# Kernel optimization log

Hardware: AMD Instinct MI355X
Metric: run time of the kernel (lower is better)

The kernel has to match this reference:

```python
import jax, jax.numpy as jnp
import numpy as np

N_HEAD = 8
T_THRESHOLD = 0.001


def setup_inputs() -> dict:
    key = jax.random.key(0)
    ks = jax.random.split(key, 5)
    B, N, NL, R = 4, 1024, 4, 256
    C = NL * R
    x = jax.random.normal(ks[0], (B, N, NL, R), dtype=jnp.float32)
    Wc = jax.random.normal(ks[1], (R, 3 * R), dtype=jnp.float32) * (1.0 / np.sqrt(R))
    bc = jnp.zeros((3 * R,), dtype=jnp.float32)
    Wp = jax.random.normal(ks[2], (C, C), dtype=jnp.float32) * (1.0 / np.sqrt(C))
    bp = jnp.zeros((C,), dtype=jnp.float32)
    return {"x": x, "Wc": Wc, "bc": bc, "Wp": Wp, "bp": bp}


def reference(x, Wc, bc, Wp, bp):
    B, N, NL, R = x.shape
    H = N_HEAD
    D = R // H  # head dim
    # shared per-level qkv projection: (B, N, NL, 3R)
    qkv = x @ Wc + bc
    q, k, v = jnp.split(qkv, 3, axis=-1)
    # split heads: (B, N, NL, H, D)
    q = q.reshape(B, N, NL, H, D)
    k = k.reshape(B, N, NL, H, D)
    v = v.reshape(B, N, NL, H, D)
    scale = 1.0 / np.sqrt(D).astype(np.float32)
    # per-level attention scores: (B, NL, H, N, N)
    att = jnp.einsum('bnlhd,bmlhd->blhnm', q, k) * scale
    att = jax.nn.softmax(att, axis=-1)
    # custom post-softmax thresholding (ReLU(softmax - T)); dropout is identity at eval
    att = jax.nn.relu(att - T_THRESHOLD)
    # multiply attentions across levels: low parent attention dooms the child
    comb = jnp.prod(att, axis=1)  # (B, H, N, N)
    # apply combined attention to each level's values: (B, N, NL, H, D)
    y = jnp.einsum('bhnm,bmlhd->bnlhd', comb, v)
    y = y.reshape(B, N, NL * H * D)  # (B, N, C)
    y = y @ Wp + bp  # c_proj; resid dropout identity at eval
    return y.reshape(B, N, NL, R)
```

## Files before the change

### kernel.cpp

```cpp
#include <hip/hip_runtime.h>

#define TTHR 0.001f
#define QSCALE 0.17677669529663687f
#define CAP 16
#define YSCALE 8388608.0f
#define YINV   1.1920928955078125e-07f

typedef _Float16 half4v __attribute__((ext_vector_type(4)));
typedef _Float16 half8v __attribute__((ext_vector_type(8)));
typedef float f32x4 __attribute__((ext_vector_type(4)));

__device__ __forceinline__ void stage_tile_s(const _Float16* __restrict__ gsrc,
                                             int rowstride, _Float16* lds, int tid)
{
  const int lane = tid & 63;
  const int w4 = (tid >> 6) << 2;
#pragma unroll
  for (int r = 0; r < 4; ++r) {
    const int p = (w4 + r) * 64 + lane;
    const int row = p >> 3, xg = p & 7;
    __builtin_amdgcn_global_load_lds(
        (const __attribute__((address_space(1))) void*)(gsrc + row * rowstride + ((xg ^ (row & 7)) << 3)),
        (__attribute__((address_space(3))) void*)(lds + (w4 + r) * 512),
        16, 0, 0);
  }
}

__global__ __launch_bounds__(256) void k_split_rm(
    const float* __restrict__ in, _Float16* __restrict__ oh,
    _Float16* __restrict__ ol, int n4)
{
  const int i = blockIdx.x * 256 + threadIdx.x;
  if (i >= n4) return;
  float4 v = ((const float4*)in)[i];
  half4v h = {(_Float16)v.x, (_Float16)v.y, (_Float16)v.z, (_Float16)v.w};
  half4v l = {(_Float16)(v.x - (float)h[0]), (_Float16)(v.y - (float)h[1]),
              (_Float16)(v.z - (float)h[2]), (_Float16)(v.w - (float)h[3])};
  ((half4v*)oh)[i] = h;
  ((half4v*)ol)[i] = l;
}

__global__ __launch_bounds__(256) void k_split_tr(
    const float* __restrict__ in, _Float16* __restrict__ oh,
    _Float16* __restrict__ ol, int K, int N)
{
  __shared__ float t[32][33];
  const int nb = N >> 5;
  const int n0 = (blockIdx.x % nb) << 5, k0 = (blockIdx.x / nb) << 5;
  const int r = threadIdx.x >> 3, c4 = (threadIdx.x & 7) << 2;
  float4 v = *(const float4*)&in[(k0 + r) * N + n0 + c4];
  t[r][c4] = v.x; t[r][c4 + 1] = v.y; t[r][c4 + 2] = v.z; t[r][c4 + 3] = v.w;
  __syncthreads();
  float a0 = t[c4][r], a1 = t[c4 + 1][r], a2 = t[c4 + 2][r], a3 = t[c4 + 3][r];
  half4v h = {(_Float16)a0, (_Float16)a1, (_Float16)a2, (_Float16)a3};
  half4v l = {(_Float16)(a0 - (float)h[0]), (_Float16)(a1 - (float)h[1]),
              (_Float16)(a2 - (float)h[2]), (_Float16)(a3 - (float)h[3])};
  *(half4v*)&oh[(n0 + r) * K + k0 + c4] = h;
  *(half4v*)&ol[(n0 + r) * K + k0 + c4] = l;
}

template<int EPI>
__global__ __launch_bounds__(256) void k_gemm_split(
    const _Float16* __restrict__ Ah, const _Float16* __restrict__ Al,
    const _Float16* __restrict__ Bh, const _Float16* __restrict__ Bl,
    const float* __restrict__ bias, int K, int kclog, int nbn,
    float* __restrict__ out, _Float16* __restrict__ Qs,
    _Float16* __restrict__ Ks, float* __restrict__ Vp)
{
  __shared__ __align__(16) _Float16 Asm[2][8192];
  __shared__ __align__(16) _Float16 Bsm[2][8192];
  const int tid = threadIdx.x, lane = tid & 63, w = tid >> 6;
  const int wr = w >> 1, wc = w & 1;
  const int lrow = lane & 15, lk = lane >> 4;
  const int mt = blockIdx.x / nbn, ct = blockIdx.x % nbn;
  const int m0 = mt << 7, c0 = ct << 7;

  const int nch = 3 << kclog;
  const int kcm = (1 << kclog) - 1;
  stage_tile_s(Ah + (size_t)m0 * K, K, Asm[0], tid);
  stage_tile_s(Bh + (size_t)c0 * K, K, Bsm[0], tid);
  __syncthreads();

  f32x4 acc[4][4] = {};
#pragma unroll 1
  for (int ch = 0; ch < nch; ++ch) {
    const int cur = ch & 1;
    if (ch + 1 < nch) {
      const int ch2 = ch + 1;
      const int phase = ch2 >> kclog, kc = ch2 & kcm;
      const _Float16* As = (phase == 2) ? Al : Ah;
      const _Float16* Bs = (phase == 1) ? Bl : Bh;
      stage_tile_s(As + (size_t)m0 * K + (kc << 6), K, Asm[cur ^ 1], tid);
      stage_tile_s(Bs + (size_t)c0 * K + (kc << 6), K, Bsm[cur ^ 1], tid);
    }
#pragma unroll
    for (int ks = 0; ks < 2; ++ks) {
      half8v af[4], bf[4];
#pragma unroll
      for (int mi = 0; mi < 4; ++mi) {
        const int row = (wr << 6) + (mi << 4) + lrow;
        const int xg = ((ks << 2) + lk) ^ (row & 7);
        af[mi] = *(const half8v*)&Asm[cur][((row << 3) + xg) << 3];
      }
#pragma unroll
      for (int ni = 0; ni < 4; ++ni) {
        const int col = (wc << 6) + (ni << 4) + lrow;
        const int xg = ((ks << 2) + lk) ^ (col & 7);
        bf[ni] = *(const half8v*)&Bsm[cur][((col << 3) + xg) << 3];
      }
#pragma unroll
      for (int mi = 0; mi < 4; ++mi)
#pragma unroll
        for (int ni = 0; ni < 4; ++ni)
          acc[mi][ni] = __builtin_amdgcn_mfma_f32_16x16x32_f16(af[mi], bf[ni], acc[mi][ni], 0, 0, 0);
    }
    __syncthreads();
  }

#pragma unroll
  for (int ni = 0; ni < 4; ++ni) {
    const int c = c0 + (wc << 6) + (ni << 4) + lrow;
    const float bv = bias[c];
    if (EPI == 0) {
#pragma unroll
      for (int mi = 0; mi < 4; ++mi)
#pragma unroll
        for (int reg = 0; reg < 4; ++reg) {
          const int m = m0 + (wr << 6) + (mi << 4) + (lk << 2) + reg;
          out[m * 1024 + c] = acc[mi][ni][reg] * YINV + bv;
        }
    } else {
      const int part = c >> 8, cc = c & 255;
      const int h = cc >> 5, d = cc & 31;
#pragma unroll
      for (int mi = 0; mi < 4; ++mi)
#pragma unroll
        for (int reg = 0; reg < 4; ++reg) {
          const int m = m0 + (wr << 6) + (mi << 4) + (lk << 2) + reg;
          const int b = m >> 12, n = (m >> 2) & 1023, l = m & 3;
          const int panel = b * 32 + l * 8 + h;
          float v = acc[mi][ni][reg] + bv;
          if (part == 2) {
            Vp[(panel << 15) + n * 32 + d] = v;
          } else {
            _Float16* dst = part ? Ks : Qs;
            if (!part) v *= QSCALE;
            _Float16 hv = (_Float16)v;
            _Float16 lv = (_Float16)(v - (float)hv);
            dst[(panel << 16) + n * 64 + d] = hv;
            dst[(panel << 16) + n * 64 + 32 + d] = lv;
          }
        }
    }
  }
}

__global__ __launch_bounds__(256) void k_score_sum(
    const _Float16* __restrict__ Qs, const _Float16* __restrict__ Ks,
    float* __restrict__ Z)
{
  __shared__ __align__(16) _Float16 Qsm[8192];
  __shared__ __align__(16) _Float16 Ksm[2][8192];
  __shared__ float Zsh[128];
  const int tid = threadIdx.x, lane = tid & 63, w = tid >> 6;
  const int wr = w >> 1, wc = w & 1;
  const int lrow = lane & 15, lk = lane >> 4;
  const int rt = blockIdx.x & 7, panel = blockIdx.x >> 3;

  stage_tile_s(Qs + (panel << 16) + (rt << 13), 64, Qsm, tid);
  stage_tile_s(Ks + (panel << 16), 64, Ksm[0], tid);
  if (tid < 128) Zsh[tid] = 0.0f;
  __syncthreads();

  const int kstA[3] = {0, 0, 4}, kstB[3] = {0, 4, 0};
  half8v af[3][4];
#pragma unroll
  for (int ks = 0; ks < 3; ++ks)
#pragma unroll
    for (int mi = 0; mi < 4; ++mi) {
      const int row = (wr << 6) + (mi << 4) + lrow;
      const int xg = (kstA[ks] + lk) ^ (row & 7);
      af[ks][mi] = *(const half8v*)&Qsm[((row << 3) + xg) << 3];
    }

  float rsum[4][4] = {};
#pragma unroll 1
  for (int ct = 0; ct < 8; ++ct) {
    const int cur = ct & 1;
    if (ct < 7)
      stage_tile_s(Ks + (panel << 16) + ((ct + 1) << 13), 64, Ksm[cur ^ 1], tid);
    f32x4 acc[4][4] = {};
#pragma unroll
    for (int ks = 0; ks < 3; ++ks) {
      half8v bf[4];
#pragma unroll
      for (int ni = 0; ni < 4; ++ni) {
        const int col = (wc << 6) + (ni << 4) + lrow;
        const int xg = (kstB[ks] + lk) ^ (col & 7);
        bf[ni] = *(const half8v*)&Ksm[cur][((col << 3) + xg) << 3];
      }
#pragma unroll
      for (int mi = 0; mi < 4; ++mi)
#pragma unroll
        for (int ni = 0; ni < 4; ++ni)
          acc[mi][ni] = __builtin_amdgcn_mfma_f32_16x16x32_f16(af[ks][mi], bf[ni], acc[mi][ni], 0, 0, 0);
    }
#pragma unroll
    for (int mi = 0; mi < 4; ++mi)
#pragma unroll
      for (int reg = 0; reg < 4; ++reg)
#pragma unroll
        for (int ni = 0; ni < 4; ++ni)
          rsum[mi][reg] += __expf(acc[mi][ni][reg]);
    __syncthreads();
  }

#pragma unroll
  for (int mi = 0; mi < 4; ++mi)
#pragma unroll
    for (int reg = 0; reg < 4; ++reg) {
      float s = rsum[mi][reg];
      s += __shfl_xor(s, 1, 64);
      s += __shfl_xor(s, 2, 64);
      s += __shfl_xor(s, 4, 64);
      s += __shfl_xor(s, 8, 64);
      if (lrow == 0) atomicAdd(&Zsh[(wr << 6) + (mi << 4) + (lk << 2) + reg], s);
    }
  __syncthreads();
  if (tid < 128) Z[panel * 1024 + (rt << 7) + tid] = Zsh[tid];
}

__global__ __launch_bounds__(256) void k_comb2(
    const _Float16* __restrict__ Qs, const _Float16* __restrict__ Ks,
    const float* __restrict__ Z, int* __restrict__ ccnt,
    unsigned short* __restrict__ cidx, float* __restrict__ cval)
{
  __shared__ __align__(16) _Float16 Asm[2][8192];
  __shared__ __align__(16) _Float16 Bsm[2][8192];
  __shared__ float tzl[2][128];
  __shared__ float rzl[128];
  __shared__ int lcnt[128];
  const int tid = threadIdx.x, lane = tid & 63, w = tid >> 6;
  const int wr = w >> 1, wc = w & 1;
  const int lrow = lane & 15, lk = lane >> 4;
  const int bid = blockIdx.x;
  const int ct = bid & 7, rt = (bid >> 3) & 7, bh = bid >> 6;
  const int b = bh >> 3, h = bh & 7;

  if (tid < 128) {
    lcnt[tid] = 0;
    const float* zp = Z + (b * 32 + h) * 1024 + (rt << 7) + tid;
    float z0 = zp[0], z1 = zp[8192], z2 = zp[16384], z3 = zp[24576];
    rzl[tid] = 1.0f / ((z0 * z1) * (z2 * z3));
    tzl[0][tid] = TTHR * z0;
  }
  {
    const int panel = b * 32 + h;
    stage_tile_s(Qs + (panel << 16) + (rt << 13), 64, Asm[0], tid);
    stage_tile_s(Ks + (panel << 16) + (ct << 13), 64, Bsm[0], tid);
  }
  __syncthreads();

  float prod[4][4][4];
#pragma unroll
  for (int mi = 0; mi < 4; ++mi)
#pragma unroll
    for (int ni = 0; ni < 4; ++ni)
#pragma unroll
      for (int r = 0; r < 4; ++r) prod[mi][ni][r] = 1.0f;

  const int kstA[3] = {0, 0, 4}, kstB[3] = {0, 4, 0};
#pragma unroll 1
  for (int l = 0; l < 4; ++l) {
    const int cur = l & 1;
    if (l < 3) {
      const int panel = b * 32 + (l + 1) * 8 + h;
      stage_tile_s(Qs + (panel << 16) + (rt << 13), 64, Asm[cur ^ 1], tid);
      stage_tile_s(Ks + (panel << 16) + (ct << 13), 64, Bsm[cur ^ 1], tid);
      if (tid < 128) tzl[cur ^ 1][tid] = TTHR * Z[panel * 1024 + (rt << 7) + tid];
    }

    f32x4 acc[4][4] = {};
#pragma unroll
    for (int ks = 0; ks < 3; ++ks) {
      half8v af[4], bf[4];
#pragma unroll
      for (int mi = 0; mi < 4; ++mi) {
        const int row = (wr << 6) + (mi << 4) + lrow;
        const int xg = (kstA[ks] + lk) ^ (row & 7);
        af[mi] = *(const half8v*)&Asm[cur][((row << 3) + xg) << 3];
      }
#pragma unroll
      for (int ni = 0; ni < 4; ++ni) {
        const int col = (wc << 6) + (ni << 4) + lrow;
        const int xg = (kstB[ks] + lk) ^ (col & 7);
        bf[ni] = *(const half8v*)&Bsm[cur][((col << 3) + xg) << 3];
      }
#pragma unroll
      for (int mi = 0; mi < 4; ++mi)
#pragma unroll
        for (int ni = 0; ni < 4; ++ni)
          acc[mi][ni] = __builtin_amdgcn_mfma_f32_16x16x32_f16(af[mi], bf[ni], acc[mi][ni], 0, 0, 0);
    }

#pragma unroll
    for (int mi = 0; mi < 4; ++mi)
#pragma unroll
      for (int reg = 0; reg < 4; ++reg) {
        const float tz = tzl[cur][(wr << 6) + (mi << 4) + (lk << 2) + reg];
#pragma unroll
        for (int ni = 0; ni < 4; ++ni) {
          const float e = __expf(acc[mi][ni][reg]) - tz;
          prod[mi][ni][reg] *= fmaxf(e, 0.0f);
        }
      }
    __syncthreads();
  }

#pragma unroll
  for (int mi = 0; mi < 4; ++mi)
#pragma unroll
    for (int ni = 0; ni < 4; ++ni)
#pragma unroll
      for (int reg = 0; reg < 4; ++reg) {
        const int rloc = (wr << 6) + (mi << 4) + (lk << 2) + reg;
        const float v = prod[mi][ni][reg] * rzl[rloc];
        if (v > 0.0f) {
          const int slot = atomicAdd(&lcnt[rloc], 1);
          if (slot < CAP) {
            const int rowc = (bh << 10) + (rt << 7) + rloc;
            const int mglob = (ct << 7) + (wc << 6) + (ni << 4) + lrow;
            cidx[(rowc * 8 + ct) * CAP + slot] = (unsigned short)mglob;
            cval[(rowc * 8 + ct) * CAP + slot] = v * YSCALE;
          }
        }
      }
  __syncthreads();
  if (tid < 128) {
    const int rowc = (bh << 10) + (rt << 7) + tid;
    ccnt[rowc * 8 + ct] = min(lcnt[tid], CAP);
  }
}

__global__ __launch_bounds__(64) void k_pv(
    const float* __restrict__ Vp, const int* __restrict__ ccnt,
    const unsigned short* __restrict__ cidx, const float* __restrict__ cval,
    _Float16* __restrict__ ysh, _Float16* __restrict__ ysl)
{
  const int rowc = blockIdx.x;
  const int bh = rowc >> 10, n = rowc & 1023;
  const int b = bh >> 3, h = bh & 7;
  const int l0 = threadIdx.x >> 5, d = threadIdx.x & 31;
  const float* vA = Vp + ((b * 32 + l0 * 8 + h) << 15) + d;
  const float* vB = vA + (16 << 15);
  float y0 = 0.f, y1 = 0.f;
  for (int mcj = 0; mcj < 8; ++mcj) {
    const int cnt = ccnt[rowc * 8 + mcj];
    const int off = (rowc * 8 + mcj) * CAP;
    for (int i = 0; i < cnt; ++i) {
      const int m = cidx[off + i];
      const float w = cval[off + i];
      y0 = fmaf(w, vA[m * 32], y0);
      y1 = fmaf(w, vB[m * 32], y1);
    }
  }
  const int idx = ((b << 10) + n) * 1024 + l0 * 256 + h * 32 + d;
  _Float16 h0 = (_Float16)y0;
  ysh[idx] = h0;
  ysl[idx] = (_Float16)(y0 - (float)h0);
  _Float16 h1 = (_Float16)y1;
  ysh[idx + 512] = h1;
  ysl[idx + 512] = (_Float16)(y1 - (float)h1);
}

extern "C" void kernel_launch(void* const* d_in, const int* in_sizes, int n_in,
                              void* d_out, int out_size, void* d_ws, size_t ws_size,
                              hipStream_t stream)
{
  const float* x  = (const float*)d_in[0];
  const float* Wc = (const float*)d_in[1];
  const float* bc = (const float*)d_in[2];
  const float* Wp = (const float*)d_in[3];
  const float* bp = (const float*)d_in[4];
  float* out = (float*)d_out;
  (void)in_sizes; (void)n_in; (void)out_size;

  if (ws_size < 98828288ull) return;
  char* wsb = (char*)d_ws;
  float*          Vp   = (float*)wsb;
  _Float16*       Qs   = (_Float16*)(wsb + 16777216);
  _Float16*       Ks   = (_Float16*)(wsb + 33554432);
  float*          Z    = (float*)(wsb + 50331648);
  _Float16*       xh   = (_Float16*)(wsb + 50855936);
  _Float16*       xl   = (_Float16*)(wsb + 59244544);
  int*            ccnt = (int*)(wsb + 67633152);
  unsigned short* cidx = (unsigned short*)(wsb + 68681728);
  float*          cval = (float*)(wsb + 77070336);
  _Float16*       Wch  = (_Float16*)(wsb + 93847552);
  _Float16*       Wcl  = (_Float16*)(wsb + 94240768);
  _Float16*       Wph  = (_Float16*)(wsb + 94633984);
  _Float16*       Wpl  = (_Float16*)(wsb + 96731136);

  k_split_rm<<<dim3(4096), dim3(256), 0, stream>>>(x, xh, xl, 1048576);
  k_split_tr<<<dim3(192), dim3(256), 0, stream>>>(Wc, Wch, Wcl, 256, 768);
  k_split_tr<<<dim3(1024), dim3(256), 0, stream>>>(Wp, Wph, Wpl, 1024, 1024);
  k_gemm_split<1><<<dim3(768), dim3(256), 0, stream>>>(
      xh, xl, Wch, Wcl, bc, 256, 2, 6, nullptr, Qs, Ks, Vp);
  k_score_sum<<<dim3(1024), dim3(256), 0, stream>>>(Qs, Ks, Z);
  k_comb2<<<dim3(2048), dim3(256), 0, stream>>>(Qs, Ks, Z, ccnt, cidx, cval);
  k_pv<<<dim3(32768), dim3(64), 0, stream>>>(Vp, ccnt, cidx, cval, xh, xl);
  k_gemm_split<0><<<dim3(256), dim3(256), 0, stream>>>(
      xh, xl, Wph, Wpl, bp, 1024, 4, 8, out, nullptr, nullptr, nullptr);
}
```

Baseline: 236.7 us.

## Halve GEMM N-tile, add XCD-aware block remap, single-buffer comb2 LDS

```diff
diff --git a/kernel.cpp b/kernel.cpp
--- a/kernel.cpp
+++ b/kernel.cpp
@@ -9,6 +9,10 @@
 typedef _Float16 half4v __attribute__((ext_vector_type(4)));
 typedef _Float16 half8v __attribute__((ext_vector_type(8)));
 typedef float f32x4 __attribute__((ext_vector_type(4)));
+
+__device__ __forceinline__ int xcd_bid() {
+  return (blockIdx.x & 7) * ((int)gridDim.x >> 3) + ((int)blockIdx.x >> 3);
+}
 
 __device__ __forceinline__ void stage_tile_s(const _Float16* __restrict__ gsrc,
                                              int rowstride, _Float16* lds, int tid)
@@ -22,6 +26,22 @@
     __builtin_amdgcn_global_load_lds(
         (const __attribute__((address_space(1))) void*)(gsrc + row * rowstride + ((xg ^ (row & 7)) << 3)),
         (__attribute__((address_space(3))) void*)(lds + (w4 + r) * 512),
+        16, 0, 0);
+  }
+}
+
+__device__ __forceinline__ void stage_tile64(const _Float16* __restrict__ gsrc,
+                                             int rowstride, _Float16* lds, int tid)
+{
+  const int lane = tid & 63;
+  const int w2 = (tid >> 6) << 1;
+#pragma unroll
+  for (int r = 0; r < 2; ++r) {
+    const int p = (w2 + r) * 64 + lane;
+    const int row = p >> 3, xg = p & 7;
+    __builtin_amdgcn_global_load_lds(
+        (const __attribute__((address_space(1))) void*)(gsrc + row * rowstride + ((xg ^ (row & 7)) << 3)),
+        (__attribute__((address_space(3))) void*)(lds + (w2 + r) * 512),
         16, 0, 0);
   }
 }
@@ -68,20 +88,21 @@
     _Float16* __restrict__ Ks, float* __restrict__ Vp)
 {
   __shared__ __align__(16) _Float16 Asm[2][8192];
-  __shared__ __align__(16) _Float16 Bsm[2][8192];
+  __shared__ __align__(16) _Float16 Bsm[2][4096];
   const int tid = threadIdx.x, lane = tid & 63, w = tid >> 6;
   const int wr = w >> 1, wc = w & 1;
   const int lrow = lane & 15, lk = lane >> 4;
-  const int mt = blockIdx.x / nbn, ct = blockIdx.x % nbn;
-  const int m0 = mt << 7, c0 = ct << 7;
+  const int bid = xcd_bid();
+  const int mt = bid / nbn, ct = bid % nbn;
+  const int m0 = mt << 7, c0 = ct << 6;
 
   const int nch = 3 << kclog;
   const int kcm = (1 << kclog) - 1;
   stage_tile_s(Ah + (size_t)m0 * K, K, Asm[0], tid);
-  stage_tile_s(Bh + (size_t)c0 * K, K, Bsm[0], tid);
-  __syncthreads();
-
-  f32x4 acc[4][4] = {};
+  stage_tile64(Bh + (size_t)c0 * K, K, Bsm[0], tid);
+  __syncthreads();
+
+  f32x4 acc[4][2] = {};
 #pragma unroll 1
   for (int ch = 0; ch < nch; ++ch) {
     const int cur = ch & 1;
@@ -91,11 +112,11 @@
       const _Float16* As = (phase == 2) ? Al : Ah;
       const _Float16* Bs = (phase == 1) ? Bl : Bh;
       stage_tile_s(As + (size_t)m0 * K + (kc << 6), K, Asm[cur ^ 1], tid);
-      stage_tile_s(Bs + (size_t)c0 * K + (kc << 6), K, Bsm[cur ^ 1], tid);
+      stage_tile64(Bs + (size_t)c0 * K + (kc << 6), K, Bsm[cur ^ 1], tid);
     }
 #pragma unroll
     for (int ks = 0; ks < 2; ++ks) {
-      half8v af[4], bf[4];
+      half8v af[4], bf[2];
 #pragma unroll
       for (int mi = 0; mi < 4; ++mi) {
         const int row = (wr << 6) + (mi << 4) + lrow;
@@ -103,23 +124,23 @@
         af[mi] = *(const half8v*)&Asm[cur][((row << 3) + xg) << 3];
       }
 #pragma unroll
-      for (int ni = 0; ni < 4; ++ni) {
-        const int col = (wc << 6) + (ni << 4) + lrow;
+      for (int ni = 0; ni < 2; ++ni) {
+        const int col = (wc << 5) + (ni << 4) + lrow;
         const int xg = ((ks << 2) + lk) ^ (col & 7);
         bf[ni] = *(const half8v*)&Bsm[cur][((col << 3) + xg) << 3];
       }
 #pragma unroll
       for (int mi = 0; mi < 4; ++mi)
 #pragma unroll
-        for (int ni = 0; ni < 4; ++ni)
+        for (int ni = 0; ni < 2; ++ni)
           acc[mi][ni] = __builtin_amdgcn_mfma_f32_16x16x32_f16(af[mi], bf[ni], acc[mi][ni], 0, 0, 0);
     }
     __syncthreads();
   }
 
 #pragma unroll
-  for (int ni = 0; ni < 4; ++ni) {
-    const int c = c0 + (wc << 6) + (ni << 4) + lrow;
+  for (int ni = 0; ni < 2; ++ni) {
+    const int c = c0 + (wc << 5) + (ni << 4) + lrow;
     const float bv = bias[c];
     if (EPI == 0) {
 #pragma unroll
@@ -165,7 +186,8 @@
   const int tid = threadIdx.x, lane = tid & 63, w = tid >> 6;
   const int wr = w >> 1, wc = w & 1;
   const int lrow = lane & 15, lk = lane >> 4;
-  const int rt = blockIdx.x & 7, panel = blockIdx.x >> 3;
+  const int bid = xcd_bid();
+  const int rt = bid & 7, panel = bid >> 3;
 
   stage_tile_s(Qs + (panel << 16) + (rt << 13), 64, Qsm, tid);
   stage_tile_s(Ks + (panel << 16), 64, Ksm[0], tid);
@@ -235,15 +257,15 @@
     const float* __restrict__ Z, int* __restrict__ ccnt,
     unsigned short* __restrict__ cidx, float* __restrict__ cval)
 {
-  __shared__ __align__(16) _Float16 Asm[2][8192];
-  __shared__ __align__(16) _Float16 Bsm[2][8192];
+  __shared__ __align__(16) _Float16 Asm[8192];
+  __shared__ __align__(16) _Float16 Bsm[8192];
   __shared__ float tzl[2][128];
   __shared__ float rzl[128];
   __shared__ int lcnt[128];
   const int tid = threadIdx.x, lane = tid & 63, w = tid >> 6;
   const int wr = w >> 1, wc = w & 1;
   const int lrow = lane & 15, lk = lane >> 4;
-  const int bid = blockIdx.x;
+  const int bid = xcd_bid();
   const int ct = bid & 7, rt = (bid >> 3) & 7, bh = bid >> 6;
   const int b = bh >> 3, h = bh & 7;
 
@@ -256,8 +278,8 @@
   }
   {
     const int panel = b * 32 + h;
-    stage_tile_s(Qs + (panel << 16) + (rt << 13), 64, Asm[0], tid);
-    stage_tile_s(Ks + (panel << 16) + (ct << 13), 64, Bsm[0], tid);
+    stage_tile_s(Qs + (panel << 16) + (rt << 13), 64, Asm, tid);
+    stage_tile_s(Ks + (panel << 16) + (ct << 13), 64, Bsm, tid);
   }
   __syncthreads();
 
@@ -272,14 +294,6 @@
   const int kstA[3] = {0, 0, 4}, kstB[3] = {0, 4, 0};
 #pragma unroll 1
   for (int l = 0; l < 4; ++l) {
-    const int cur = l & 1;
-    if (l < 3) {
-      const int panel = b * 32 + (l + 1) * 8 + h;
-      stage_tile_s(Qs + (panel << 16) + (rt << 13), 64, Asm[cur ^ 1], tid);
-      stage_tile_s(Ks + (panel << 16) + (ct << 13), 64, Bsm[cur ^ 1], tid);
-      if (tid < 128) tzl[cur ^ 1][tid] = TTHR * Z[panel * 1024 + (rt << 7) + tid];
-    }
-
     f32x4 acc[4][4] = {};
 #pragma unroll
     for (int ks = 0; ks < 3; ++ks) {
@@ -288,13 +302,13 @@
       for (int mi = 0; mi < 4; ++mi) {
         const int row = (wr << 6) + (mi << 4) + lrow;
         const int xg = (kstA[ks] + lk) ^ (row & 7);
-        af[mi] = *(const half8v*)&Asm[cur][((row << 3) + xg) << 3];
+        af[mi] = *(const half8v*)&Asm[((row << 3) + xg) << 3];
       }
 #pragma unroll
       for (int ni = 0; ni < 4; ++ni) {
         const int col = (wc << 6) + (ni << 4) + lrow;
         const int xg = (kstB[ks] + lk) ^ (col & 7);
-        bf[ni] = *(const half8v*)&Bsm[cur][((col << 3) + xg) << 3];
+        bf[ni] = *(const half8v*)&Bsm[((col << 3) + xg) << 3];
       }
 #pragma unroll
       for (int mi = 0; mi < 4; ++mi)
@@ -302,19 +316,25 @@
         for (int ni = 0; ni < 4; ++ni)
           acc[mi][ni] = __builtin_amdgcn_mfma_f32_16x16x32_f16(af[mi], bf[ni], acc[mi][ni], 0, 0, 0);
     }
-
+    __syncthreads();
+    if (l < 3) {
+      const int panel = b * 32 + (l + 1) * 8 + h;
+      stage_tile_s(Qs + (panel << 16) + (rt << 13), 64, Asm, tid);
+      stage_tile_s(Ks + (panel << 16) + (ct << 13), 64, Bsm, tid);
+      if (tid < 128) tzl[(l + 1) & 1][tid] = TTHR * Z[panel * 1024 + (rt << 7) + tid];
+    }
 #pragma unroll
     for (int mi = 0; mi < 4; ++mi)
 #pragma unroll
       for (int reg = 0; reg < 4; ++reg) {
-        const float tz = tzl[cur][(wr << 6) + (mi << 4) + (lk << 2) + reg];
+        const float tz = tzl[l & 1][(wr << 6) + (mi << 4) + (lk << 2) + reg];
 #pragma unroll
         for (int ni = 0; ni < 4; ++ni) {
           const float e = __expf(acc[mi][ni][reg]) - tz;
           prod[mi][ni][reg] *= fmaxf(e, 0.0f);
         }
       }
-    __syncthreads();
+    if (l < 3) __syncthreads();
   }
 
 #pragma unroll
@@ -404,11 +424,11 @@
   k_split_rm<<<dim3(4096), dim3(256), 0, stream>>>(x, xh, xl, 1048576);
   k_split_tr<<<dim3(192), dim3(256), 0, stream>>>(Wc, Wch, Wcl, 256, 768);
   k_split_tr<<<dim3(1024), dim3(256), 0, stream>>>(Wp, Wph, Wpl, 1024, 1024);
-  k_gemm_split<1><<<dim3(768), dim3(256), 0, stream>>>(
-      xh, xl, Wch, Wcl, bc, 256, 2, 6, nullptr, Qs, Ks, Vp);
+  k_gemm_split<1><<<dim3(1536), dim3(256), 0, stream>>>(
+      xh, xl, Wch, Wcl, bc, 256, 2, 12, nullptr, Qs, Ks, Vp);
   k_score_sum<<<dim3(1024), dim3(256), 0, stream>>>(Qs, Ks, Z);
   k_comb2<<<dim3(2048), dim3(256), 0, stream>>>(Qs, Ks, Z, ccnt, cidx, cval);
   k_pv<<<dim3(32768), dim3(64), 0, stream>>>(Vp, ccnt, cidx, cval, xh, xl);
-  k_gemm_split<0><<<dim3(256), dim3(256), 0, stream>>>(
-      xh, xl, Wph, Wpl, bp, 1024, 4, 8, out, nullptr, nullptr, nullptr);
-}
+  k_gemm_split<0><<<dim3(512), dim3(256), 0, stream>>>(
+      xh, xl, Wph, Wpl, bp, 1024, 4, 16, out, nullptr, nullptr, nullptr);
+}
```

After: 264.9 us. 11.9% more time.
